# Kernel tuning notes

Measured on AMD Instinct MI355X. Metric: run time of the kernel, lower is better.

Reference implementation:

```python
import jax, jax.numpy as jnp
import numpy as np

HIDDEN = 1024
HEAD = 64
B, T = 4, 4096

def setup_inputs() -> dict:
    key = jax.random.key(0)
    kx, kq, kk, kv = jax.random.split(key, 4)
    bound = 1.0 / np.sqrt(HIDDEN)  # nn.Linear default init range
    x = jax.random.normal(kx, (B, T, HIDDEN), dtype=jnp.float32)
    W_Q = jax.random.uniform(kq, (HIDDEN, HEAD), jnp.float32, -bound, bound)
    W_K = jax.random.uniform(kk, (HIDDEN, HEAD), jnp.float32, -bound, bound)
    W_V = jax.random.uniform(kv, (HIDDEN, HEAD), jnp.float32, -bound, bound)
    return {"x": x, "W_Q": W_Q, "W_K": W_K, "W_V": W_V}

def reference(x, W_Q, W_K, W_V):
    # Q,K,V: [B,T,HEAD]
    Q = x @ W_Q
    K = x @ W_K
    V = x @ W_V
    scale = 1.0 / np.sqrt(HEAD).astype(np.float32)
    scores = jnp.einsum('bqd,bkd->bqk', Q, K) * scale  # [B,T,T]
    Tlen = x.shape[1]
    causal = jnp.tril(jnp.ones((Tlen, Tlen), dtype=bool))
    scores = jnp.where(causal, scores, -jnp.inf)
    attn = jax.nn.softmax(scores, axis=-1)
    # dropout=0.0 -> identity
    return jnp.einsum('bqk,bkd->bqd', attn, V)
```

## Files before the change

### kernel.cpp

```cpp
#include <hip/hip_runtime.h>

typedef short bf16x8 __attribute__((ext_vector_type(8)));
typedef float f32x4 __attribute__((ext_vector_type(4)));

#define T_LEN 4096
#define NB    4
#define HID   1024
#define HD    64

__device__ __forceinline__ unsigned short f2bf(float f) {
    union { float f; unsigned int u; } v; v.f = f;
    unsigned int u = v.u;
    u += 0x7fffu + ((u >> 16) & 1u);
    return (unsigned short)(u >> 16);
}

__global__ __launch_bounds__(256) void wtrans_kernel(
    const float* __restrict__ wq, const float* __restrict__ wk,
    const float* __restrict__ wv, unsigned short* __restrict__ Wpk)
{
    const int idx = blockIdx.x * 256 + threadIdx.x;
    const int k = idx & 1023;
    const int n = idx >> 10;
    const float* w = (n < 64) ? wq : ((n < 128) ? wk : wv);
    const int ks = k >> 5, g = (k >> 3) & 3, j = k & 7;
    const int nt = n >> 4, lr = n & 15;
    const int lane = g * 16 + lr;
    Wpk[((size_t)(ks * 12 + nt) << 9) + (lane << 3) + j] =
        f2bf(w[(size_t)k * 64 + (n & 63)]);
}

__global__ __launch_bounds__(256, 4) void qkv_proj_kernel(
    const float* __restrict__ x, const unsigned short* __restrict__ Wpk,
    unsigned short* __restrict__ Qb, unsigned short* __restrict__ Kpk,
    unsigned short* __restrict__ Vpk)
{
    __shared__ float red[3][16][193];
    const int tid = threadIdx.x;
    const int kq = tid >> 6, lane = tid & 63;
    const int g = lane >> 4, lr = lane & 15;
    const int t0 = blockIdx.x * 16;

    f32x4 acc[12];
#pragma unroll
    for (int i = 0; i < 12; ++i) acc[i] = (f32x4)(0.0f);

    const float* xrow = x + (size_t)(t0 + lr) * HID;
#pragma unroll 4
    for (int s = 0; s < 8; ++s) {
        const int ks = kq * 8 + s;
        const float4 a0 = *(const float4*)(xrow + ks * 32 + g * 8);
        const float4 a1 = *(const float4*)(xrow + ks * 32 + g * 8 + 4);
        bf16x8 af;
        af[0] = (short)f2bf(a0.x); af[1] = (short)f2bf(a0.y);
        af[2] = (short)f2bf(a0.z); af[3] = (short)f2bf(a0.w);
        af[4] = (short)f2bf(a1.x); af[5] = (short)f2bf(a1.y);
        af[6] = (short)f2bf(a1.z); af[7] = (short)f2bf(a1.w);
        const unsigned short* wp = Wpk + (((size_t)ks * 12) << 9) + (lane << 3);
#pragma unroll
        for (int nt = 0; nt < 12; ++nt) {
            const bf16x8 bfr = *(const bf16x8*)(wp + ((size_t)nt << 9));
            acc[nt] = __builtin_amdgcn_mfma_f32_16x16x32_bf16(af, bfr, acc[nt], 0, 0, 0);
        }
    }

    if (kq != 0) {
#pragma unroll
        for (int nt = 0; nt < 12; ++nt)
#pragma unroll
            for (int r = 0; r < 4; ++r)
                red[kq - 1][g * 4 + r][nt * 16 + lr] = acc[nt][r];
    }
    __syncthreads();
    if (kq == 0) {
#pragma unroll
        for (int nt = 0; nt < 12; ++nt)
#pragma unroll
            for (int r = 0; r < 4; ++r)
                acc[nt][r] += red[0][g * 4 + r][nt * 16 + lr]
                            + red[1][g * 4 + r][nt * 16 + lr]
                            + red[2][g * 4 + r][nt * 16 + lr];

        const int rowb = t0 + g * 4;
        const int bb = t0 >> 12;
        const size_t bpk = (size_t)bb * (T_LEN * HD);
#pragma unroll
        for (int nt = 0; nt < 4; ++nt)
#pragma unroll
            for (int r = 0; r < 4; ++r)
                Qb[(size_t)(rowb + r) * HD + nt * 16 + lr] = f2bf(acc[nt][r]);
#pragma unroll
        for (int nt = 0; nt < 4; ++nt)
#pragma unroll
            for (int r = 0; r < 4; ++r) {
                const int tl = (rowb + r) & 4095;
                const int d  = nt * 16 + lr;
                Kpk[bpk + ((((tl >> 4) * 8 + (d >> 3)) * 16 + (tl & 15)) << 3) + (d & 7)]
                    = f2bf(acc[nt + 4][r]);
            }
#pragma unroll
        for (int nt = 0; nt < 4; ++nt)
#pragma unroll
            for (int r = 0; r < 4; ++r) {
                const int tl = (rowb + r) & 4095;
                const int d  = nt * 16 + lr;
                Vpk[bpk + (((tl >> 3) * 64 + d) << 3) + (tl & 7)] = f2bf(acc[nt + 8][r]);
            }
    }
}

#define MOFF 96.0f

__device__ __forceinline__ void kv_pair(
    const int t0, const int lane, const int g, const int lr,
    const unsigned short* __restrict__ kpk_b, const unsigned short* __restrict__ vpk_b,
    unsigned short (*P)[136],
    const bf16x8 qf0, const bf16x8 qf1,
    f32x4 oacc[4], float lrow[4])
{
    const float SCL = 0.18033688011112042f;
    f32x4 s[8];
    const unsigned short* kbase = kpk_b + (((size_t)(t0 >> 4)) << 10) + (lane << 3);
#pragma unroll
    for (int nt = 0; nt < 8; ++nt) {
        const bf16x8 kf0 = *(const bf16x8*)(kbase + ((size_t)nt << 10));
        const bf16x8 kf1 = *(const bf16x8*)(kbase + ((size_t)nt << 10) + 512);
        f32x4 a = (f32x4)(0.0f);
        a = __builtin_amdgcn_mfma_f32_16x16x32_bf16(qf0, kf0, a, 0, 0, 0);
        a = __builtin_amdgcn_mfma_f32_16x16x32_bf16(qf1, kf1, a, 0, 0, 0);
        s[nt] = a;
    }
#pragma unroll
    for (int nt = 0; nt < 8; ++nt)
#pragma unroll
        for (int r = 0; r < 4; ++r) {
            const float p = __builtin_amdgcn_exp2f((s[nt][r] - MOFF) * SCL);
            lrow[r] += p;
            P[g * 4 + r][nt * 16 + lr] = f2bf(p);
        }

    const bf16x8 pf0 = *(const bf16x8*)&P[lr][g * 8];
    const bf16x8 pf1 = *(const bf16x8*)&P[lr][32 + g * 8];
    const bf16x8 pf2 = *(const bf16x8*)&P[lr][64 + g * 8];
    const bf16x8 pf3 = *(const bf16x8*)&P[lr][96 + g * 8];
    const unsigned short* vb = vpk_b + (((size_t)((t0 >> 3) + g)) << 9) + (lr << 3);
#pragma unroll
    for (int dt = 0; dt < 4; ++dt) {
        const bf16x8 vf0 = *(const bf16x8*)(vb + dt * 128);
        const bf16x8 vf1 = *(const bf16x8*)(vb + (4 << 9) + dt * 128);
        const bf16x8 vf2 = *(const bf16x8*)(vb + (8 << 9) + dt * 128);
        const bf16x8 vf3 = *(const bf16x8*)(vb + (12 << 9) + dt * 128);
        oacc[dt] = __builtin_amdgcn_mfma_f32_16x16x32_bf16(pf0, vf0, oacc[dt], 0, 0, 0);
        oacc[dt] = __builtin_amdgcn_mfma_f32_16x16x32_bf16(pf1, vf1, oacc[dt], 0, 0, 0);
        oacc[dt] = __builtin_amdgcn_mfma_f32_16x16x32_bf16(pf2, vf2, oacc[dt], 0, 0, 0);
        oacc[dt] = __builtin_amdgcn_mfma_f32_16x16x32_bf16(pf3, vf3, oacc[dt], 0, 0, 0);
    }
}

template <bool MASKED>
__device__ __forceinline__ void kv_single(
    const int t0, const int qw0, const int lane, const int g, const int lr,
    const unsigned short* __restrict__ kpk_b, const unsigned short* __restrict__ vpk_b,
    unsigned short (*P)[136],
    const bf16x8 qf0, const bf16x8 qf1,
    f32x4 oacc[4], float lrow[4])
{
    const float SCL = 0.18033688011112042f;
    f32x4 s[4];
    const unsigned short* kbase = kpk_b + (((size_t)(t0 >> 4)) << 10) + (lane << 3);
#pragma unroll
    for (int nt = 0; nt < 4; ++nt) {
        const bf16x8 kf0 = *(const bf16x8*)(kbase + ((size_t)nt << 10));
        const bf16x8 kf1 = *(const bf16x8*)(kbase + ((size_t)nt << 10) + 512);
        f32x4 a = (f32x4)(0.0f);
        a = __builtin_amdgcn_mfma_f32_16x16x32_bf16(qf0, kf0, a, 0, 0, 0);
        a = __builtin_amdgcn_mfma_f32_16x16x32_bf16(qf1, kf1, a, 0, 0, 0);
        s[nt] = a;
    }
    if (MASKED) {
#pragma unroll
        for (int nt = 0; nt < 4; ++nt) {
            const int kj = t0 + nt * 16 + lr;
#pragma unroll
            for (int r = 0; r < 4; ++r)
                if (kj > qw0 + g * 4 + r) s[nt][r] = -3.0e38f;
        }
    }
#pragma unroll
    for (int nt = 0; nt < 4; ++nt)
#pragma unroll
        for (int r = 0; r < 4; ++r) {
            const float p = __builtin_amdgcn_exp2f((s[nt][r] - MOFF) * SCL);
            lrow[r] += p;
            P[g * 4 + r][nt * 16 + lr] = f2bf(p);
        }

    const bf16x8 pf0 = *(const bf16x8*)&P[lr][g * 8];
    const bf16x8 pf1 = *(const bf16x8*)&P[lr][32 + g * 8];
    const unsigned short* vb = vpk_b + (((size_t)((t0 >> 3) + g)) << 9) + (lr << 3);
#pragma unroll
    for (int dt = 0; dt < 4; ++dt) {
        const bf16x8 vf0 = *(const bf16x8*)(vb + dt * 128);
        const bf16x8 vf1 = *(const bf16x8*)(vb + (4 << 9) + dt * 128);
        oacc[dt] = __builtin_amdgcn_mfma_f32_16x16x32_bf16(pf0, vf0, oacc[dt], 0, 0, 0);
        oacc[dt] = __builtin_amdgcn_mfma_f32_16x16x32_bf16(pf1, vf1, oacc[dt], 0, 0, 0);
    }
}

__global__ __launch_bounds__(64) void attn_part_kernel(
    const unsigned short* __restrict__ Qb, const unsigned short* __restrict__ Kpk,
    const unsigned short* __restrict__ Vpk,
    float* __restrict__ Opart, float* __restrict__ Lpart)
{
    int i = blockIdx.x;
    const int b = i / 1152;
    i -= b * 1152;
    int c = 0, rem = i;
#pragma unroll
    for (int cc = 0; cc < 8; ++cc) {
        const int cnt = 256 - (cc << 5);
        if (c == cc && rem >= cnt) { rem -= cnt; c = cc + 1; }
    }
    const int qt = (c << 5) + rem;

    __shared__ unsigned short Plds[16][136];
    const int lane = threadIdx.x & 63;
    const int g = lane >> 4, lr = lane & 15;
    const int qw0 = qt << 4;
    const int kvbase = c << 9;

    const unsigned short* qp = Qb + (size_t)((b << 12) + qw0 + lr) * HD + g * 8;
    const bf16x8 qf0 = *(const bf16x8*)qp;
    const bf16x8 qf1 = *(const bf16x8*)(qp + 32);
    const unsigned short* kpk_b = Kpk + (size_t)b * (T_LEN * HD);
    const unsigned short* vpk_b = Vpk + (size_t)b * (T_LEN * HD);

    f32x4 oacc[4];
#pragma unroll
    for (int i2 = 0; i2 < 4; ++i2) oacc[i2] = (f32x4)(0.0f);
    float lrow[4] = {0.f, 0.f, 0.f, 0.f};

    const bool diag = ((qt >> 5) == c);
    const int nfull = diag ? ((qw0 - kvbase + 1) >> 6) : 8;
    int it = 0;
    for (; it + 2 <= nfull; it += 2)
        kv_pair(kvbase + it * 64, lane, g, lr, kpk_b, vpk_b, Plds, qf0, qf1, oacc, lrow);
    if (it < nfull)
        kv_single<false>(kvbase + it * 64, qw0, lane, g, lr, kpk_b, vpk_b, Plds,
                         qf0, qf1, oacc, lrow);
    if (diag)
        kv_single<true>(kvbase + nfull * 64, qw0, lane, g, lr, kpk_b, vpk_b, Plds,
                        qf0, qf1, oacc, lrow);

#pragma unroll
    for (int m = 1; m < 16; m <<= 1)
#pragma unroll
        for (int r = 0; r < 4; ++r) lrow[r] += __shfl_xor(lrow[r], m, 64);

    const size_t p = ((size_t)((b << 8) + qt) << 3) + c;
    float* Op = Opart + (p << 10);
    float* Lp = Lpart + (p << 4);
#pragma unroll
    for (int r = 0; r < 4; ++r) {
        const int wrow = g * 4 + r;
        if (lr == 0) Lp[wrow] = lrow[r];
#pragma unroll
        for (int dt = 0; dt < 4; ++dt)
            Op[wrow * 64 + dt * 16 + lr] = oacc[dt][r];
    }
}

__global__ __launch_bounds__(256) void attn_merge_kernel(
    const float* __restrict__ Opart, const float* __restrict__ Lpart,
    float* __restrict__ out)
{
    const int qt = blockIdx.x & 255, b = blockIdx.x >> 8;
    const int nch = (qt >> 5) + 1;
    const int t = threadIdx.x;
    const int row = t >> 4, d0 = (t & 15) << 2;
    const size_t pb = (size_t)blockIdx.x << 3;

    float L = 0.f;
#pragma unroll
    for (int c = 0; c < 8; ++c)
        if (c < nch) L += Lpart[((pb + c) << 4) + row];
    const float inv = 1.0f / L;

    f32x4 o = (f32x4)(0.0f);
#pragma unroll
    for (int c = 0; c < 8; ++c) {
        if (c < nch) {
            const f32x4 v = *(const f32x4*)(Opart + (((pb + c) << 4) + row) * 64 + d0);
#pragma unroll
            for (int j = 0; j < 4; ++j) o[j] += v[j];
        }
    }
    f32x4 res;
#pragma unroll
    for (int j = 0; j < 4; ++j) res[j] = o[j] * inv;
    *(f32x4*)(out + (size_t)((b << 12) + (qt << 4) + row) * HD + d0) = res;
}

extern "C" void kernel_launch(void* const* d_in, const int* in_sizes, int n_in,
                              void* d_out, int out_size, void* d_ws, size_t ws_size,
                              hipStream_t stream) {
    const float* x  = (const float*)d_in[0];
    const float* wq = (const float*)d_in[1];
    const float* wk = (const float*)d_in[2];
    const float* wv = (const float*)d_in[3];
    float* out = (float*)d_out;

    float* Opart = (float*)d_ws;
    float* Lpart = Opart + ((size_t)8192 * 1024);
    unsigned short* Qb  = (unsigned short*)(Lpart + (size_t)8192 * 16);
    unsigned short* Kpk = Qb  + (size_t)NB * T_LEN * HD;
    unsigned short* Vpk = Kpk + (size_t)NB * T_LEN * HD;
    unsigned short* Wpk = Vpk + (size_t)NB * T_LEN * HD;

    wtrans_kernel<<<768, 256, 0, stream>>>(wq, wk, wv, Wpk);
    qkv_proj_kernel<<<1024, 256, 0, stream>>>(x, Wpk, Qb, Kpk, Vpk);
    attn_part_kernel<<<NB * 1152, 64, 0, stream>>>(Qb, Kpk, Vpk, Opart, Lpart);
    attn_merge_kernel<<<NB * 256, 256, 0, stream>>>(Opart, Lpart, out);
}
```

Before: 72.80 us.

## Restructure QKV projection with double-buffered LDS staging and 2x2 wave tiling

```diff
diff --git a/kernel.cpp b/kernel.cpp
--- a/kernel.cpp
+++ b/kernel.cpp
@@ -13,6 +13,12 @@
     unsigned int u = v.u;
     u += 0x7fffu + ((u >> 16) & 1u);
     return (unsigned short)(u >> 16);
+}
+
+__device__ __forceinline__ void gl_lds16(const float* g, float* l) {
+    __builtin_amdgcn_global_load_lds(
+        (const __attribute__((address_space(1))) unsigned int*)g,
+        (__attribute__((address_space(3))) unsigned int*)l, 16, 0, 0);
 }
 
 __global__ __launch_bounds__(256) void wtrans_kernel(
@@ -30,82 +36,71 @@
         f2bf(w[(size_t)k * 64 + (n & 63)]);
 }
 
-__global__ __launch_bounds__(256, 4) void qkv_proj_kernel(
+__global__ __launch_bounds__(256, 2) void qkv_proj_kernel(
     const float* __restrict__ x, const unsigned short* __restrict__ Wpk,
     unsigned short* __restrict__ Qb, unsigned short* __restrict__ Kpk,
     unsigned short* __restrict__ Vpk)
 {
-    __shared__ float red[3][16][193];
+    __shared__ __align__(16) float xs[2][1024];
     const int tid = threadIdx.x;
-    const int kq = tid >> 6, lane = tid & 63;
+    const int w = tid >> 6, lane = tid & 63;
     const int g = lane >> 4, lr = lane & 15;
-    const int t0 = blockIdx.x * 16;
-
-    f32x4 acc[12];
-#pragma unroll
-    for (int i = 0; i < 12; ++i) acc[i] = (f32x4)(0.0f);
-
-    const float* xrow = x + (size_t)(t0 + lr) * HID;
-#pragma unroll 4
-    for (int s = 0; s < 8; ++s) {
-        const int ks = kq * 8 + s;
-        const float4 a0 = *(const float4*)(xrow + ks * 32 + g * 8);
-        const float4 a1 = *(const float4*)(xrow + ks * 32 + g * 8 + 4);
+    const int t0 = blockIdx.x * 32;
+    const int mh = w & 1, nh = w >> 1;
+    const int arow = mh * 16 + lr;
+    const int rx = lr & 7;
+
+    const int srow = (w << 3) + (lane >> 3);
+    const int schunk = (lane & 7) ^ (lane >> 3);
+    const float* gstage = x + (size_t)(t0 + srow) * HID + (schunk << 2);
+    const int ldst = w << 8;
+
+    f32x4 acc[6];
+#pragma unroll
+    for (int i = 0; i < 6; ++i) acc[i] = (f32x4)(0.0f);
+
+    gl_lds16(gstage, &xs[0][ldst]);
+    __syncthreads();
+
+    for (int t = 0; t < 32; ++t) {
+        const int cur = t & 1;
+        if (t < 31) gl_lds16(gstage + (t + 1) * 32, &xs[cur ^ 1][ldst]);
+
+        const float4 a0 = *(const float4*)&xs[cur][arow * 32 + (((g * 2) ^ rx) << 2)];
+        const float4 a1 = *(const float4*)&xs[cur][arow * 32 + (((g * 2 + 1) ^ rx) << 2)];
         bf16x8 af;
         af[0] = (short)f2bf(a0.x); af[1] = (short)f2bf(a0.y);
         af[2] = (short)f2bf(a0.z); af[3] = (short)f2bf(a0.w);
         af[4] = (short)f2bf(a1.x); af[5] = (short)f2bf(a1.y);
         af[6] = (short)f2bf(a1.z); af[7] = (short)f2bf(a1.w);
-        const unsigned short* wp = Wpk + (((size_t)ks * 12) << 9) + (lane << 3);
-#pragma unroll
-        for (int nt = 0; nt < 12; ++nt) {
-            const bf16x8 bfr = *(const bf16x8*)(wp + ((size_t)nt << 9));
-            acc[nt] = __builtin_amdgcn_mfma_f32_16x16x32_bf16(af, bfr, acc[nt], 0, 0, 0);
-        }
-    }
-
-    if (kq != 0) {
-#pragma unroll
-        for (int nt = 0; nt < 12; ++nt)
-#pragma unroll
-            for (int r = 0; r < 4; ++r)
-                red[kq - 1][g * 4 + r][nt * 16 + lr] = acc[nt][r];
-    }
-    __syncthreads();
-    if (kq == 0) {
-#pragma unroll
-        for (int nt = 0; nt < 12; ++nt)
-#pragma unroll
-            for (int r = 0; r < 4; ++r)
-                acc[nt][r] += red[0][g * 4 + r][nt * 16 + lr]
-                            + red[1][g * 4 + r][nt * 16 + lr]
-                            + red[2][g * 4 + r][nt * 16 + lr];
-
-        const int rowb = t0 + g * 4;
-        const int bb = t0 >> 12;
-        const size_t bpk = (size_t)bb * (T_LEN * HD);
-#pragma unroll
-        for (int nt = 0; nt < 4; ++nt)
-#pragma unroll
-            for (int r = 0; r < 4; ++r)
-                Qb[(size_t)(rowb + r) * HD + nt * 16 + lr] = f2bf(acc[nt][r]);
-#pragma unroll
-        for (int nt = 0; nt < 4; ++nt)
-#pragma unroll
-            for (int r = 0; r < 4; ++r) {
-                const int tl = (rowb + r) & 4095;
-                const int d  = nt * 16 + lr;
-                Kpk[bpk + ((((tl >> 4) * 8 + (d >> 3)) * 16 + (tl & 15)) << 3) + (d & 7)]
-                    = f2bf(acc[nt + 4][r]);
+
+        const unsigned short* wp = Wpk + (((size_t)(t * 12 + nh * 6)) << 9) + (lane << 3);
+#pragma unroll
+        for (int j = 0; j < 6; ++j) {
+            const bf16x8 bfr = *(const bf16x8*)(wp + ((size_t)j << 9));
+            acc[j] = __builtin_amdgcn_mfma_f32_16x16x32_bf16(af, bfr, acc[j], 0, 0, 0);
+        }
+        __syncthreads();
+    }
+
+    const size_t bpk = (size_t)(t0 >> 12) * (T_LEN * HD);
+#pragma unroll
+    for (int j = 0; j < 6; ++j) {
+        const int nt = nh * 6 + j;
+#pragma unroll
+        for (int r = 0; r < 4; ++r) {
+            const int grow = t0 + mh * 16 + g * 4 + r;
+            const unsigned short val = f2bf(acc[j][r]);
+            if (nt < 4) {
+                Qb[(size_t)grow * HD + nt * 16 + lr] = val;
+            } else if (nt < 8) {
+                const int tl = grow & 4095, d = (nt - 4) * 16 + lr;
+                Kpk[bpk + ((((tl >> 4) * 8 + (d >> 3)) * 16 + (tl & 15)) << 3) + (d & 7)] = val;
+            } else {
+                const int tl = grow & 4095, d = (nt - 8) * 16 + lr;
+                Vpk[bpk + (((tl >> 3) * 64 + d) << 3) + (tl & 7)] = val;
             }
-#pragma unroll
-        for (int nt = 0; nt < 4; ++nt)
-#pragma unroll
-            for (int r = 0; r < 4; ++r) {
-                const int tl = (rowb + r) & 4095;
-                const int d  = nt * 16 + lr;
-                Vpk[bpk + (((tl >> 3) * 64 + d) << 3) + (tl & 7)] = f2bf(acc[nt + 8][r]);
-            }
+        }
     }
 }
 
@@ -318,7 +313,7 @@
     unsigned short* Wpk = Vpk + (size_t)NB * T_LEN * HD;
 
     wtrans_kernel<<<768, 256, 0, stream>>>(wq, wk, wv, Wpk);
-    qkv_proj_kernel<<<1024, 256, 0, stream>>>(x, Wpk, Qb, Kpk, Vpk);
+    qkv_proj_kernel<<<512, 256, 0, stream>>>(x, Wpk, Qb, Kpk, Vpk);
     attn_part_kernel<<<NB * 1152, 64, 0, stream>>>(Qb, Kpk, Vpk, Opart, Lpart);
     attn_merge_kernel<<<NB * 256, 256, 0, stream>>>(Opart, Lpart, out);
 }
```

Measured after the change: 75.06 us. +3.1%, slower.
